# Kernel tuning notes

Hardware: AMD Instinct MI355X
Metric: run time of the kernel (lower is better)

Reference implementation:

```python
import jax, jax.numpy as jnp
import numpy as np

B, C1, C2 = 8, 256, 256
Cc = 128          # c = int(c2 * e)
RED = 16          # reduction in FrequencyModulation
HEADS = 8
HD = Cc // HEADS  # 16
HH, WW = 32, 32


def _c1x1(x, w, b=None):
    # 1x1 conv as channel contraction; w: [out_c, in_c]
    y = jnp.einsum('bchw,oc->bohw', x, w)
    return y if b is None else y + b[None, :, None, None]


def setup_inputs() -> dict:
    key = jax.random.key(0)
    ks = jax.random.split(key, 22)
    s = 0.02
    p = {}
    p['x'] = jax.random.normal(ks[0], (B, C1, HH, WW), jnp.float32)
    p['cv1_w'] = jax.random.normal(ks[1], (2 * Cc, C1), jnp.float32) * s
    p['cv1_b'] = jnp.zeros((2 * Cc,), jnp.float32)
    # FrequencyModulation params
    p['fm_w1'] = jax.random.normal(ks[2], (Cc // RED, Cc), jnp.float32) * s
    p['fm_w2'] = jax.random.normal(ks[3], (Cc, Cc // RED), jnp.float32) * s
    p['ca_w1'] = jax.random.normal(ks[4], (Cc // RED, Cc), jnp.float32) * s
    p['ca_w2'] = jax.random.normal(ks[5], (Cc, Cc // RED), jnp.float32) * s
    # TokenStatisticsSelfAttention params (qkv_bias=False)
    p['qkv_w'] = jax.random.normal(ks[6], (3 * Cc, Cc), jnp.float32) * s
    p['tproj_w'] = jax.random.normal(ks[7], (Cc, Cc), jnp.float32) * s
    p['tproj_b'] = jnp.zeros((Cc,), jnp.float32)
    # SpatialQuantizedRouter params
    p['dw_w'] = jax.random.normal(ks[8], (Cc, 1, 3, 3), jnp.float32) * s  # depthwise
    p['dw_b'] = jnp.zeros((Cc,), jnp.float32)
    p['rt_w'] = jax.random.normal(ks[9], (1, Cc), jnp.float32) * s
    p['rt_b'] = jnp.zeros((1,), jnp.float32)
    p['q_w'] = jax.random.normal(ks[10], (Cc, Cc), jnp.float32) * s
    p['k_w'] = jax.random.normal(ks[11], (Cc, Cc), jnp.float32) * s
    p['v_w'] = jax.random.normal(ks[12], (Cc, Cc), jnp.float32) * s
    p['sproj_w'] = jax.random.normal(ks[13], (Cc, Cc), jnp.float32) * s
    p['sproj_b'] = jnp.zeros((Cc,), jnp.float32)
    p['cv2_w'] = jax.random.normal(ks[14], (C2, 3 * Cc), jnp.float32) * s
    p['cv2_b'] = jnp.zeros((C2,), jnp.float32)
    return p


def _forward(x, cv1_w, cv1_b, fm_w1, fm_w2, ca_w1, ca_w2, qkv_w, tproj_w,
             tproj_b, dw_w, dw_b, rt_w, rt_b, q_w, k_w, v_w, sproj_w,
             sproj_b, cv2_w, cv2_b):
    Bb, _, H, W = x.shape
    N = H * W
    y = _c1x1(x, cv1_w, cv1_b)
    y0, y1 = y[:, :Cc], y[:, Cc:]

    # ---- Branch 1: FrequencyModulation ----
    xf = jnp.fft.rfft2(y1.astype(jnp.float32), norm='ortho')  # [B,c,H,W//2+1] complex
    mag = jnp.abs(xf)
    pooled = mag.mean(axis=(-2, -1))                          # [B,c]
    fw = jax.nn.sigmoid(jax.nn.relu(pooled @ fm_w1.T) @ fm_w2.T)  # [B,c]
    # mag*fw*exp(i*phase) == fw * xf  (fw is real, per batch/channel)
    xs = jnp.fft.irfft2(xf * fw[:, :, None, None].astype(jnp.complex64),
                        s=(H, W), norm='ortho')               # [B,c,H,W]
    ca = jax.nn.sigmoid(jax.nn.relu(xs.mean(axis=(-2, -1)) @ ca_w1.T) @ ca_w2.T)
    freq_out = xs * ca[:, :, None, None]

    # ---- Branch 2: TokenStatisticsSelfAttention ----
    xt = y1.reshape(Bb, Cc, N).transpose(0, 2, 1)             # [B,N,c]
    qkv = (xt @ qkv_w.T).reshape(Bb, N, 3, HEADS, HD).transpose(2, 0, 3, 1, 4)
    q, k, v = qkv[0], qkv[1], qkv[2]                          # [B,h,N,d]
    var_v = jnp.var(v, axis=-1, ddof=1, keepdims=True)        # [B,h,N,1] (unbiased)
    var_k = jnp.var(k, axis=-1, ddof=1, keepdims=True)
    attn = jax.nn.softmax(jnp.einsum('bhnx,bhmx->bhnm', var_v, var_k) * (HD ** -0.5), axis=-1)
    to = jnp.einsum('bhnm,bhmd->bhnd', attn, v).transpose(0, 2, 1, 3).reshape(Bb, N, Cc)
    stat_out = ((to @ tproj_w.T) + tproj_b).transpose(0, 2, 1).reshape(Bb, Cc, H, W)

    # ---- Branch 3: SpatialQuantizedRouter (training-mode blend) ----
    x_local = jax.lax.conv_general_dilated(
        y1, dw_w, (1, 1), 'SAME', feature_group_count=Cc,
        dimension_numbers=('NCHW', 'OIHW', 'NCHW')) + dw_b[None, :, None, None]
    p_route = jax.nn.sigmoid(y1.mean(axis=(-2, -1)) @ rt_w.T + rt_b)  # [B,1]
    qb = jnp.sign(_c1x1(y1, q_w).reshape(Bb, Cc, N))
    kb = jnp.sign(_c1x1(y1, k_w).reshape(Bb, Cc, N))
    vv = _c1x1(y1, v_w).reshape(Bb, Cc, N)
    a2 = jax.nn.softmax(jnp.einsum('bcn,bcm->bnm', qb, kb) * (Cc ** -0.5), axis=-1)
    # torch: bmm(v, attn.T) -> out[b,c,n] = sum_m v[b,c,m]*attn[b,n,m]
    ob = jnp.einsum('bcm,bnm->bcn', vv, a2).reshape(Bb, Cc, H, W)
    out_bin = _c1x1(ob, sproj_w, sproj_b)
    alpha = p_route.reshape(Bb, 1, 1, 1)
    spat_out = (1.0 - alpha) * x_local + alpha * out_bin

    attn_out = freq_out + stat_out + spat_out
    yc = jnp.concatenate([y0, y1, attn_out], axis=1)          # [B,3c,H,W]
    out = _c1x1(yc, cv2_w, cv2_b)
    return x + out  # add: shortcut and c1 == c2


def reference(x, cv1_w, cv1_b, fm_w1, fm_w2, ca_w1, ca_w2, qkv_w, tproj_w,
              tproj_b, dw_w, dw_b, rt_w, rt_b, q_w, k_w, v_w, sproj_w,
              sproj_b, cv2_w, cv2_b):
    return _forward(x, cv1_w, cv1_b, fm_w1, fm_w2, ca_w1, ca_w2, qkv_w,
                    tproj_w, tproj_b, dw_w, dw_b, rt_w, rt_b, q_w, k_w, v_w,
                    sproj_w, sproj_b, cv2_w, cv2_b)
```

## Files before the change

### kernel.cpp

```cpp
#include <hip/hip_runtime.h>
#include <math.h>

#define BATCH 8
#define NPIX 1024

typedef __attribute__((ext_vector_type(8))) short short8v;
typedef __attribute__((ext_vector_type(4))) float f32x4;

__device__ inline unsigned short f2bf(float x) {
  unsigned int u = __float_as_uint(x);
  return (unsigned short)((u + 0x7FFFu + ((u >> 16) & 1u)) >> 16);
}
__device__ inline float bf2f(unsigned short h) {
  return __uint_as_float((unsigned int)h << 16);
}
__device__ inline unsigned long long pack4bf(float a, float b, float c, float d) {
  return (unsigned long long)(unsigned short)f2bf(a) |
         ((unsigned long long)(unsigned short)f2bf(b) << 16) |
         ((unsigned long long)(unsigned short)f2bf(c) << 32) |
         ((unsigned long long)(unsigned short)f2bf(d) << 48);
}

__global__ __launch_bounds__(256) void convw_kernel(
    const float* __restrict__ cv1_w, const float* __restrict__ qkv_w,
    const float* __restrict__ tproj_w, const float* __restrict__ sproj_w,
    const float* __restrict__ cv2_w, const float* __restrict__ q_w,
    const float* __restrict__ k_w, const float* __restrict__ v_w,
    short* __restrict__ wb) {
  int i = blockIdx.x * 256 + threadIdx.x;
  float v;
  if (i < 65536) v = cv1_w[i];
  else if (i < 163840) {
    int j = i - 65536;
    if (j < 49152) v = qkv_w[j];
    else {
      int jj = j - 49152, wsel = jj >> 14, r = jj & 16383;
      v = (wsel == 0) ? q_w[r] : (wsel == 1) ? k_w[r] : v_w[r];
    }
  }
  else if (i < 180224) v = tproj_w[i - 163840];
  else if (i < 196608) v = sproj_w[i - 180224];
  else v = cv2_w[i - 196608];
  wb[i] = (short)f2bf(v);
}

template<int MODE, bool HAS_BIAS, bool HAS_RES, bool XF32T, bool EMIT_HI>
__global__ __launch_bounds__(256) void mgemm_kernel(
    const short* __restrict__ Wb, const void* __restrict__ Xsrc, int ldx,
    const float* __restrict__ bias, const float* __restrict__ res,
    void* __restrict__ Y0, void* __restrict__ Y1,
    int K, long sXT, long sY, long sR, int tStride, int tOff) {
  __shared__ __align__(16) short As[64][40];
  __shared__ __align__(16) short Bs[64][40];
  const int b = blockIdx.z;
  const int n0 = blockIdx.x * 64, m0 = blockIdx.y * 64;
  const int tid = threadIdx.x;
  const int l = tid & 63, w = tid >> 6;
  const int wm = w >> 1, wn = w & 1;
  const int sr = tid >> 2, sko = (tid & 3) * 8;
  const int xr = tid >> 3, xcg = (tid & 7) * 8;
  const int fr = l & 15, fk = (l >> 4) * 8;
  f32x4 acc[2][2] = {};
  for (int k0 = 0; k0 < K; k0 += 32) {
    *(uint4*)&As[sr][sko] = *(const uint4*)(Wb + (long)(m0 + sr) * K + k0 + sko);
    if (XF32T) {
      const float* Xf = (const float*)Xsrc + (long)b * sXT;
      const float4 xa = *(const float4*)(Xf + (long)(k0 + xr) * 1024 + n0 + xcg);
      const float4 xb = *(const float4*)(Xf + (long)(k0 + xr) * 1024 + n0 + xcg + 4);
      Bs[xcg + 0][xr] = (short)f2bf(xa.x); Bs[xcg + 1][xr] = (short)f2bf(xa.y);
      Bs[xcg + 2][xr] = (short)f2bf(xa.z); Bs[xcg + 3][xr] = (short)f2bf(xa.w);
      Bs[xcg + 4][xr] = (short)f2bf(xb.x); Bs[xcg + 5][xr] = (short)f2bf(xb.y);
      Bs[xcg + 6][xr] = (short)f2bf(xb.z); Bs[xcg + 7][xr] = (short)f2bf(xb.w);
    } else {
      const short* Xb = (const short*)Xsrc + (long)b * sXT;
      *(uint4*)&Bs[sr][sko] = *(const uint4*)(Xb + (long)(n0 + sr) * ldx + k0 + sko);
    }
    __syncthreads();
    short8v a0 = *(short8v*)&As[wm * 32 + fr][fk];
    short8v a1 = *(short8v*)&As[wm * 32 + 16 + fr][fk];
    short8v b0 = *(short8v*)&Bs[wn * 32 + fr][fk];
    short8v b1 = *(short8v*)&Bs[wn * 32 + 16 + fr][fk];
    acc[0][0] = __builtin_amdgcn_mfma_f32_16x16x32_bf16(a0, b0, acc[0][0], 0, 0, 0);
    acc[0][1] = __builtin_amdgcn_mfma_f32_16x16x32_bf16(a0, b1, acc[0][1], 0, 0, 0);
    acc[1][0] = __builtin_amdgcn_mfma_f32_16x16x32_bf16(a1, b0, acc[1][0], 0, 0, 0);
    acc[1][1] = __builtin_amdgcn_mfma_f32_16x16x32_bf16(a1, b1, acc[1][1], 0, 0, 0);
    __syncthreads();
  }
#pragma unroll
  for (int tm = 0; tm < 2; tm++) {
    const int m_base = m0 + wm * 32 + tm * 16 + (l >> 4) * 4;
#pragma unroll
    for (int tn = 0; tn < 2; tn++) {
      const int n = n0 + wn * 32 + tn * 16 + (l & 15);
      float v0 = acc[tm][tn][0], v1 = acc[tm][tn][1];
      float v2 = acc[tm][tn][2], v3 = acc[tm][tn][3];
      if (HAS_BIAS) {
        v0 += bias[m_base]; v1 += bias[m_base + 1];
        v2 += bias[m_base + 2]; v3 += bias[m_base + 3];
      }
      if (HAS_RES) {
        v0 += res[(long)b * sR + (long)(m_base + 0) * 1024 + n];
        v1 += res[(long)b * sR + (long)(m_base + 1) * 1024 + n];
        v2 += res[(long)b * sR + (long)(m_base + 2) * 1024 + n];
        v3 += res[(long)b * sR + (long)(m_base + 3) * 1024 + n];
      }
      if (MODE == 0) {
        float* Y = (float*)Y0 + (long)b * sY + n;
        Y[(long)(m_base + 0) * 1024] = v0; Y[(long)(m_base + 1) * 1024] = v1;
        Y[(long)(m_base + 2) * 1024] = v2; Y[(long)(m_base + 3) * 1024] = v3;
      } else if (MODE == 1) {
        short* Y = (short*)Y0 + (long)b * sY + n;
        Y[(long)(m_base + 0) * 1024] = (short)f2bf(v0);
        Y[(long)(m_base + 1) * 1024] = (short)f2bf(v1);
        Y[(long)(m_base + 2) * 1024] = (short)f2bf(v2);
        Y[(long)(m_base + 3) * 1024] = (short)f2bf(v3);
      } else if (MODE == 2) {
        *(unsigned long long*)((short*)Y0 + ((long)b * 1024 + n) * tStride +
                               tOff + m_base) = pack4bf(v0, v1, v2, v3);
        if (EMIT_HI && m_base >= 128) {
          float* Y = (float*)Y1 + ((long)b * 128 + m_base - 128) * 1024 + n;
          Y[0] = v0; Y[1024] = v1; Y[2048] = v2; Y[3072] = v3;
        }
      } else {
        if (m0 < 384) {
          float* Y = (float*)Y0 + (long)b * 384 * 1024 + (long)m_base * 1024 + n;
          Y[0] = v0; Y[1024] = v1; Y[2048] = v2; Y[3072] = v3;
        } else {
          *(unsigned long long*)((short*)Y1 + ((long)b * 1024 + n) * 384 +
                                 (m_base - 384)) = pack4bf(v0, v1, v2, v3);
        }
      }
    }
  }
}

__global__ __launch_bounds__(256) void fftpool_kernel(
    const float* __restrict__ y1, float* __restrict__ pooled, float* __restrict__ m1) {
  const int bc = blockIdx.x;
  const float* img = y1 + (long)bc * NPIX;
  __shared__ float im[1024];
  __shared__ float Gr[32][17], Gi[32][17];
  __shared__ float cs[32], sn[32];
  __shared__ float red[256];
  const int t = threadIdx.x;
  if (t < 32) {
    float ang = -0.19634954084936207f * (float)t;
    __sincosf(ang, &sn[t], &cs[t]);
  }
  float lsum = 0.f;
  for (int i = t; i < 1024; i += 256) { float v = img[i]; im[i] = v; lsum += v; }
  red[t] = lsum;
  __syncthreads();
  for (int s = 128; s > 0; s >>= 1) {
    if (t < s) red[t] += red[t + s];
    __syncthreads();
  }
  if (t == 0) m1[bc] = red[0] * (1.f / 1024.f);
  for (int i = t; i < 544; i += 256) {
    int h = i / 17, v = i % 17;
    float ar = 0.f, ai = 0.f;
    for (int w2 = 0; w2 < 32; w2++) {
      int k = (v * w2) & 31;
      float x = im[h * 32 + w2];
      ar += x * cs[k]; ai += x * sn[k];
    }
    Gr[h][v] = ar; Gi[h][v] = ai;
  }
  __syncthreads();
  float asum = 0.f;
  for (int i = t; i < 544; i += 256) {
    int u = i / 17, v = i % 17;
    float xr = 0.f, xi = 0.f;
    for (int h = 0; h < 32; h++) {
      int k = (u * h) & 31;
      float gr = Gr[h][v], gi = Gi[h][v];
      xr += gr * cs[k] - gi * sn[k];
      xi += gr * sn[k] + gi * cs[k];
    }
    asum += sqrtf(xr * xr + xi * xi);
  }
  red[t] = asum;
  __syncthreads();
  for (int s = 128; s > 0; s >>= 1) {
    if (t < s) red[t] += red[t + s];
    __syncthreads();
  }
  if (t == 0) pooled[bc] = red[0] * (1.f / (32.f * 544.f));
}

__global__ __launch_bounds__(128) void gates_kernel(
    const float* __restrict__ pooled, const float* __restrict__ m1,
    const float* __restrict__ fm_w1, const float* __restrict__ fm_w2,
    const float* __restrict__ ca_w1, const float* __restrict__ ca_w2,
    const float* __restrict__ rt_w, const float* __restrict__ rt_b,
    float* __restrict__ g, float* __restrict__ alpha) {
  const int b = blockIdx.x, t = threadIdx.x;
  __shared__ float h1[8], fwv[128], xsm[128], h2[8];
  const float* pb = pooled + b * 128;
  const float* mb = m1 + b * 128;
  if (t < 8) {
    float s = 0.f;
    for (int c = 0; c < 128; c++) s += pb[c] * fm_w1[t * 128 + c];
    h1[t] = fmaxf(s, 0.f);
  }
  __syncthreads();
  {
    float s = 0.f;
    for (int r = 0; r < 8; r++) s += h1[r] * fm_w2[t * 8 + r];
    float fw = 1.f / (1.f + __expf(-s));
    fwv[t] = fw; xsm[t] = fw * mb[t];
  }
  __syncthreads();
  if (t < 8) {
    float s = 0.f;
    for (int c = 0; c < 128; c++) s += xsm[c] * ca_w1[t * 128 + c];
    h2[t] = fmaxf(s, 0.f);
  }
  __syncthreads();
  {
    float s = 0.f;
    for (int r = 0; r < 8; r++) s += h2[r] * ca_w2[t * 8 + r];
    float ca = 1.f / (1.f + __expf(-s));
    g[b * 128 + t] = fwv[t] * ca;
  }
  if (t == 0) {
    float s = 0.f;
    for (int c = 0; c < 128; c++) s += mb[c] * rt_w[c];
    s += rt_b[0];
    alpha[b] = 1.f / (1.f + __expf(-s));
  }
}

__global__ __launch_bounds__(256) void varmax_kernel(
    const float* __restrict__ qkvb, float* __restrict__ var_k,
    float* __restrict__ var_v, float* __restrict__ maxvk,
    short* __restrict__ vTb) {
  const int bh = blockIdx.x;
  const int b = bh >> 3, h = bh & 7;
  __shared__ float red[256];
  __shared__ float trans[16][256];
  const float* kb = qkvb + ((long)b * 384 + 128 + h * 16) * NPIX;
  const float* vb = qkvb + ((long)b * 384 + 256 + h * 16) * NPIX;
  float mx = 0.f;
  for (int j = 0; j < 4; j++) {
    int n = threadIdx.x + j * 256;
    float xk[16], xv[16], sk = 0.f, sv = 0.f;
#pragma unroll
    for (int d = 0; d < 16; d++) {
      xk[d] = kb[(long)d * NPIX + n]; sk += xk[d];
      xv[d] = vb[(long)d * NPIX + n]; sv += xv[d];
    }
    float mk = sk * (1.f / 16.f), mv = sv * (1.f / 16.f);
    float vk_ = 0.f, vv_ = 0.f;
#pragma unroll
    for (int d = 0; d < 16; d++) {
      float a = xk[d] - mk; vk_ += a * a;
      float c = xv[d] - mv; vv_ += c * c;
    }
    vk_ *= (1.f / 15.f); vv_ *= (1.f / 15.f);
    var_k[(long)bh * NPIX + n] = vk_;
    var_v[(long)bh * NPIX + n] = vv_;
    mx = fmaxf(mx, vk_);
#pragma unroll
    for (int d = 0; d < 16; d++) trans[d][threadIdx.x] = xv[d];
    __syncthreads();
    {
      int d = threadIdx.x >> 4, mc = threadIdx.x & 15;
      __align__(16) short tmp[16];
#pragma unroll
      for (int e = 0; e < 16; e++) tmp[e] = (short)f2bf(trans[d][mc * 16 + e]);
      short* dst = vTb + ((long)bh * 16 + d) * 1024 + j * 256 + mc * 16;
      *(uint4*)dst = *(uint4*)tmp;
      *(uint4*)(dst + 8) = *(uint4*)(tmp + 8);
    }
    __syncthreads();
  }
  red[threadIdx.x] = mx;
  __syncthreads();
  for (int s = 128; s > 0; s >>= 1) {
    if (threadIdx.x < s) red[threadIdx.x] = fmaxf(red[threadIdx.x], red[threadIdx.x + s]);
    __syncthreads();
  }
  if (threadIdx.x == 0) maxvk[bh] = red[0];
}

__global__ __launch_bounds__(256) void stat_mfma_kernel(
    const short* __restrict__ vTb, const float* __restrict__ var_k,
    const float* __restrict__ var_v, const float* __restrict__ maxvk,
    short* __restrict__ tcT) {
  const int bh = blockIdx.x;
  const int b = bh >> 3, h = bh & 7;
  const int n0 = blockIdx.y * 64;
  const int tid = threadIdx.x;
  const int l = tid & 63, w = tid >> 6;
  const int ln = l & 15, lk = l >> 4;
  const int n = n0 + w * 16 + ln;
  __shared__ float vk[1024];
  for (int i = tid; i < 1024; i += 256) vk[i] = var_k[(long)bh * 1024 + i];
  const float cn = var_v[(long)bh * 1024 + n] * 0.25f;
  const float mv = maxvk[bh];
  const short* arow = vTb + ((long)bh * 16 + ln) * 1024 + lk * 8;
  __syncthreads();
  f32x4 acc = {};
  float psum = 0.f;
  for (int m0 = 0; m0 < 1024; m0 += 32) {
    short8v afrag = *(const short8v*)(arow + m0);
    short8v bfrag;
#pragma unroll
    for (int j = 0; j < 8; j++) {
      float wv = __expf(cn * (vk[m0 + lk * 8 + j] - mv));
      psum += wv;
      bfrag[j] = (short)f2bf(wv);
    }
    acc = __builtin_amdgcn_mfma_f32_16x16x32_bf16(afrag, bfrag, acc, 0, 0, 0);
  }
  psum += __shfl_xor(psum, 16);
  psum += __shfl_xor(psum, 32);
  const float inv = 1.f / psum;
  *(unsigned long long*)(tcT + ((long)b * 1024 + n) * 128 + h * 16 + lk * 4) =
      pack4bf(acc[0] * inv, acc[1] * inv, acc[2] * inv, acc[3] * inv);
}

__global__ __launch_bounds__(256) void pack_kernel(
    const short* __restrict__ sqkvT,
    unsigned long long* __restrict__ qbits, unsigned long long* __restrict__ kbits) {
  const int wave = threadIdx.x >> 6, lane = threadIdx.x & 63;
  const long p = (long)blockIdx.x * 4 + wave;
  const short* base = sqkvT + p * 384;
  unsigned long long q0 = __ballot(bf2f((unsigned short)base[lane]) > 0.f);
  unsigned long long q1 = __ballot(bf2f((unsigned short)base[64 + lane]) > 0.f);
  unsigned long long k0 = __ballot(bf2f((unsigned short)base[128 + lane]) > 0.f);
  unsigned long long k1 = __ballot(bf2f((unsigned short)base[192 + lane]) > 0.f);
  if (lane == 0) {
    qbits[p * 2] = q0; qbits[p * 2 + 1] = q1;
    kbits[p * 2] = k0; kbits[p * 2 + 1] = k1;
  }
}

__global__ __launch_bounds__(256) void obgemm_kernel(
    const short* __restrict__ pvb, const unsigned long long* __restrict__ qbits,
    const unsigned long long* __restrict__ kbits, short* __restrict__ pnum,
    float* __restrict__ pden) {
  const int b = blockIdx.z;
  const int sp = blockIdx.y;
  const int n0 = blockIdx.x * 64;
  const int kb0 = sp * 256;
  __shared__ __align__(16) short As[128][40];
  __shared__ __align__(16) unsigned long long kbsh[256][2];
  const int tid = threadIdx.x;
  const int l = tid & 63, w = tid >> 6;
  const int ln = l & 15, lk = l >> 4;
  const int n = n0 + w * 16 + ln;
  const unsigned long long q0 = qbits[((long)b * 1024 + n) * 2];
  const unsigned long long q1 = qbits[((long)b * 1024 + n) * 2 + 1];
  *(uint4*)&kbsh[tid][0] = *(const uint4*)(kbits + ((long)b * 1024 + kb0 + tid) * 2);
  const float fs = 0.08838834764831845f;
  const int sc = tid >> 1, sh = (tid & 1) * 16;
  const short* pvrow = pvb + ((long)b * 128 + sc) * 1024 + kb0;
  f32x4 acc[8] = {};
  float psum = 0.f;
  for (int ks = 0; ks < 8; ks++) {
    *(uint4*)&As[sc][sh] = *(const uint4*)(pvrow + ks * 32 + sh);
    *(uint4*)&As[sc][sh + 8] = *(const uint4*)(pvrow + ks * 32 + sh + 8);
    __syncthreads();
    const int mloc = ks * 32 + lk * 8;
    short8v bfrag;
#pragma unroll
    for (int j = 0; j < 8; j++) {
      unsigned long long kw0 = kbsh[mloc + j][0];
      unsigned long long kw1 = kbsh[mloc + j][1];
      int ham = __popcll(kw0 ^ q0) + __popcll(kw1 ^ q1);
      float wv = __expf((float)(128 - 2 * ham) * fs);
      psum += wv;
      bfrag[j] = (short)f2bf(wv);
    }
#pragma unroll
    for (int ct = 0; ct < 8; ct++) {
      short8v afrag = *(short8v*)&As[ct * 16 + ln][lk * 8];
      acc[ct] = __builtin_amdgcn_mfma_f32_16x16x32_bf16(afrag, bfrag, acc[ct], 0, 0, 0);
    }
    __syncthreads();
  }
  short* dst = pnum + (((long)sp * 8 + b) * 128) * 1024 + n;
#pragma unroll
  for (int ct = 0; ct < 8; ct++)
#pragma unroll
    for (int i = 0; i < 4; i++)
      dst[(long)(ct * 16 + lk * 4 + i) * 1024] = (short)f2bf(acc[ct][i]);
  psum += __shfl_xor(psum, 16);
  psum += __shfl_xor(psum, 32);
  if (lk == 0)
    pden[((long)sp * 8 + b) * 1024 + n] = psum;
}

__global__ __launch_bounds__(256) void dwcombine_kernel(
    const float* __restrict__ y1, float* __restrict__ attn,
    const float* __restrict__ dw_w, const float* __restrict__ dw_b,
    const short* __restrict__ pnum, const float* __restrict__ pden,
    const float* __restrict__ sproj_b, const float* __restrict__ g,
    const float* __restrict__ alpha) {
  const int bc = blockIdx.x;
  const int b = bc >> 7, cx = bc & 127;
  const float* img = y1 + (long)bc * NPIX;
  float* dst = attn + (long)bc * NPIX;
  float w[9];
#pragma unroll
  for (int i = 0; i < 9; i++) w[i] = dw_w[cx * 9 + i];
  const float bias = dw_b[cx];
  const float a = alpha[b];
  const float gg = g[bc];
  const float sb = sproj_b[cx];
  const long ns = 8L * 128 * 1024;
  const long ds = 8L * 1024;
  const long nbase = (long)bc * 1024;
  const long dbase = (long)b * 1024;
  for (int i = threadIdx.x; i < 1024; i += 256) {
    int h = i >> 5, wx = i & 31;
    float s = bias;
#pragma unroll
    for (int ky = 0; ky < 3; ky++) {
      int hh = h + ky - 1;
      if (hh < 0 || hh > 31) continue;
#pragma unroll
      for (int kx = 0; kx < 3; kx++) {
        int ww2 = wx + kx - 1;
        if (ww2 < 0 || ww2 > 31) continue;
        s += img[hh * 32 + ww2] * w[ky * 3 + kx];
      }
    }
    float num = bf2f((unsigned short)pnum[nbase + i]) +
                bf2f((unsigned short)pnum[nbase + i + ns]) +
                bf2f((unsigned short)pnum[nbase + i + 2 * ns]) +
                bf2f((unsigned short)pnum[nbase + i + 3 * ns]);
    float den = pden[dbase + i] + pden[dbase + i + ds] +
                pden[dbase + i + 2 * ds] + pden[dbase + i + 3 * ds];
    float obv = num / den + sb;
    dst[i] = gg * img[i] + (1.f - a) * s + a * obv;
  }
}

extern "C" void kernel_launch(void* const* d_in, const int* in_sizes, int n_in,
                              void* d_out, int out_size, void* d_ws, size_t ws_size,
                              hipStream_t stream) {
  const float* x = (const float*)d_in[0];
  const float* cv1_w = (const float*)d_in[1];
  const float* cv1_b = (const float*)d_in[2];
  const float* fm_w1 = (const float*)d_in[3];
  const float* fm_w2 = (const float*)d_in[4];
  const float* ca_w1 = (const float*)d_in[5];
  const float* ca_w2 = (const float*)d_in[6];
  const float* qkv_w = (const float*)d_in[7];
  const float* tproj_w = (const float*)d_in[8];
  const float* tproj_b = (const float*)d_in[9];
  const float* dw_w = (const float*)d_in[10];
  const float* dw_b = (const float*)d_in[11];
  const float* rt_w = (const float*)d_in[12];
  const float* rt_b = (const float*)d_in[13];
  const float* q_w = (const float*)d_in[14];
  const float* k_w = (const float*)d_in[15];
  const float* v_w = (const float*)d_in[16];
  const float* sproj_w = (const float*)d_in[17];
  const float* sproj_b = (const float*)d_in[18];
  const float* cv2_w = (const float*)d_in[19];
  const float* cv2_b = (const float*)d_in[20];
  float* out = (float*)d_out;

  char* wsp = (char*)d_ws;
  size_t off = 0;
  auto alloc = [&](size_t bytes) {
    void* p = wsp + off;
    off += (bytes + 255) & ~(size_t)255;
    return p;
  };
  float* qkvb = (float*)alloc(8UL * 384 * 1024 * 4);
  float* y1 = (float*)alloc(8UL * 128 * 1024 * 4);
  float* attn = (float*)alloc(8UL * 128 * 1024 * 4);
  short* ycT = (short*)alloc(8UL * 1024 * 384 * 2);
  short* sqkvT = (short*)alloc(8UL * 1024 * 384 * 2);
  short* tcT = (short*)alloc(8UL * 1024 * 128 * 2);
  short* pvb = (short*)alloc(8UL * 128 * 1024 * 2);
  short* wb = (short*)alloc(294912UL * 2);
  short* vTb = (short*)alloc(64UL * 16 * 1024 * 2);
  float* pden = (float*)alloc(4UL * 8 * 1024 * 4);
  float* var_k = (float*)alloc(8UL * 8 * 1024 * 4);
  float* var_v = (float*)alloc(8UL * 8 * 1024 * 4);
  float* maxvk = (float*)alloc(64 * 4);
  float* pooled = (float*)alloc(1024 * 4);
  float* m1 = (float*)alloc(1024 * 4);
  float* g = (float*)alloc(1024 * 4);
  float* alpha = (float*)alloc(8 * 4);
  unsigned long long* qbits = (unsigned long long*)alloc(8192UL * 2 * 8);
  unsigned long long* kbits = (unsigned long long*)alloc(8192UL * 2 * 8);
  short* pnum = (short*)qkvb;
  const short* cv1b = wb;
  const short* qsb = wb + 65536;
  const short* tprojb = wb + 163840;
  const short* sprojb = wb + 180224;
  const short* cv2b = wb + 196608;
  if (off > ws_size) return;

  dim3 blk(256);
  convw_kernel<<<dim3(1152), blk, 0, stream>>>(cv1_w, qkv_w, tproj_w, sproj_w,
                                               cv2_w, q_w, k_w, v_w, wb);
  mgemm_kernel<2, true, false, true, true><<<dim3(16, 4, 8), blk, 0, stream>>>(
      cv1b, x, 0, cv1_b, nullptr, ycT, y1, 256, 256L * 1024, 0, 0, 384, 0);
  fftpool_kernel<<<dim3(1024), blk, 0, stream>>>(y1, pooled, m1);
  gates_kernel<<<dim3(8), dim3(128), 0, stream>>>(pooled, m1, fm_w1, fm_w2,
                                                  ca_w1, ca_w2, rt_w, rt_b, g, alpha);
  mgemm_kernel<3, false, false, false, false><<<dim3(16, 12, 8), blk, 0, stream>>>(
      qsb, ycT + 128, 384, nullptr, nullptr, qkvb, sqkvT, 128, 1024L * 384,
      0, 0, 0, 0);
  varmax_kernel<<<dim3(64), blk, 0, stream>>>(qkvb, var_k, var_v, maxvk, vTb);
  stat_mfma_kernel<<<dim3(64, 16), blk, 0, stream>>>(vTb, var_k, var_v, maxvk, tcT);
  pack_kernel<<<dim3(2048), blk, 0, stream>>>(sqkvT, qbits, kbits);
  mgemm_kernel<1, false, false, false, false><<<dim3(16, 2, 8), blk, 0, stream>>>(
      sprojb, sqkvT + 256, 384, nullptr, nullptr, pvb, nullptr, 128,
      1024L * 384, 128L * 1024, 0, 0, 0);
  obgemm_kernel<<<dim3(16, 4, 8), blk, 0, stream>>>(pvb, qbits, kbits, pnum, pden);
  dwcombine_kernel<<<dim3(1024), blk, 0, stream>>>(y1, attn, dw_w, dw_b, pnum,
                                                   pden, sproj_b, g, alpha);
  mgemm_kernel<2, true, true, false, false><<<dim3(16, 2, 8), blk, 0, stream>>>(
      tprojb, tcT, 128, tproj_b, attn, ycT, nullptr, 128, 1024L * 128, 0,
      128L * 1024, 384, 256);
  mgemm_kernel<0, true, true, false, false><<<dim3(16, 4, 8), blk, 0, stream>>>(
      cv2b, ycT, 384, cv2_b, x, out, nullptr, 384, 1024L * 384, 256L * 1024,
      256L * 1024, 0, 0);
}
```

Measured before the change: 123.0 us.

## Fuse weight conversion, depthwise combine, and split varmax across more blocks

Removes the standalone weight-conversion kernel. Most GEMMs now convert fp32 weights to bf16 while loading tiles, and the qkv/q/k/v conversion is folded into the FFT pooling kernel. The depthwise-conv and attention-combine kernel is fused into the epilogue of the tproj GEMM, which drops the fp32 attn intermediate and one launch. varmax is split into 4 chunks per head with an atomicMax reduction, and gates_kernel zeroes the max buffer. The cost is redundant per-tile weight conversion, a heavier epilogue doing scattered 3x3 loads, and reliance on atomicMax over float bits, which is valid only because variances are non-negative.

```diff
diff --git a/kernel.cpp b/kernel.cpp
--- a/kernel.cpp
+++ b/kernel.cpp
@@ -21,35 +21,16 @@
          ((unsigned long long)(unsigned short)f2bf(d) << 48);
 }
 
-__global__ __launch_bounds__(256) void convw_kernel(
-    const float* __restrict__ cv1_w, const float* __restrict__ qkv_w,
-    const float* __restrict__ tproj_w, const float* __restrict__ sproj_w,
-    const float* __restrict__ cv2_w, const float* __restrict__ q_w,
-    const float* __restrict__ k_w, const float* __restrict__ v_w,
-    short* __restrict__ wb) {
-  int i = blockIdx.x * 256 + threadIdx.x;
-  float v;
-  if (i < 65536) v = cv1_w[i];
-  else if (i < 163840) {
-    int j = i - 65536;
-    if (j < 49152) v = qkv_w[j];
-    else {
-      int jj = j - 49152, wsel = jj >> 14, r = jj & 16383;
-      v = (wsel == 0) ? q_w[r] : (wsel == 1) ? k_w[r] : v_w[r];
-    }
-  }
-  else if (i < 180224) v = tproj_w[i - 163840];
-  else if (i < 196608) v = sproj_w[i - 180224];
-  else v = cv2_w[i - 196608];
-  wb[i] = (short)f2bf(v);
-}
-
-template<int MODE, bool HAS_BIAS, bool HAS_RES, bool XF32T, bool EMIT_HI>
+template<int MODE, bool HAS_BIAS, bool HAS_RES, bool XF32T, bool WF32, bool EMIT_HI>
 __global__ __launch_bounds__(256) void mgemm_kernel(
-    const short* __restrict__ Wb, const void* __restrict__ Xsrc, int ldx,
+    const void* __restrict__ Wsrc, const void* __restrict__ Xsrc, int ldx,
     const float* __restrict__ bias, const float* __restrict__ res,
     void* __restrict__ Y0, void* __restrict__ Y1,
-    int K, long sXT, long sY, long sR, int tStride, int tOff) {
+    int K, long sXT, long sY, long sR, int tStride, int tOff,
+    const float* __restrict__ y1p, const short* __restrict__ pnumS,
+    const float* __restrict__ pdenP, const float* __restrict__ sproj_bP,
+    const float* __restrict__ dw_wP, const float* __restrict__ dw_bP,
+    const float* __restrict__ gP, const float* __restrict__ alphaP) {
   __shared__ __align__(16) short As[64][40];
   __shared__ __align__(16) short Bs[64][40];
   const int b = blockIdx.z;
@@ -62,7 +43,18 @@
   const int fr = l & 15, fk = (l >> 4) * 8;
   f32x4 acc[2][2] = {};
   for (int k0 = 0; k0 < K; k0 += 32) {
-    *(uint4*)&As[sr][sko] = *(const uint4*)(Wb + (long)(m0 + sr) * K + k0 + sko);
+    if (WF32) {
+      const float* Wf = (const float*)Wsrc;
+      const float4 wa = *(const float4*)(Wf + (long)(m0 + sr) * K + k0 + sko);
+      const float4 wbv = *(const float4*)(Wf + (long)(m0 + sr) * K + k0 + sko + 4);
+      As[sr][sko + 0] = (short)f2bf(wa.x); As[sr][sko + 1] = (short)f2bf(wa.y);
+      As[sr][sko + 2] = (short)f2bf(wa.z); As[sr][sko + 3] = (short)f2bf(wa.w);
+      As[sr][sko + 4] = (short)f2bf(wbv.x); As[sr][sko + 5] = (short)f2bf(wbv.y);
+      As[sr][sko + 6] = (short)f2bf(wbv.z); As[sr][sko + 7] = (short)f2bf(wbv.w);
+    } else {
+      *(uint4*)&As[sr][sko] =
+          *(const uint4*)((const short*)Wsrc + (long)(m0 + sr) * K + k0 + sko);
+    }
     if (XF32T) {
       const float* Xf = (const float*)Xsrc + (long)b * sXT;
       const float4 xa = *(const float4*)(Xf + (long)(k0 + xr) * 1024 + n0 + xcg);
@@ -121,7 +113,7 @@
           float* Y = (float*)Y1 + ((long)b * 128 + m_base - 128) * 1024 + n;
           Y[0] = v0; Y[1024] = v1; Y[2048] = v2; Y[3072] = v3;
         }
-      } else {
+      } else if (MODE == 3) {
         if (m0 < 384) {
           float* Y = (float*)Y0 + (long)b * 384 * 1024 + (long)m_base * 1024 + n;
           Y[0] = v0; Y[1024] = v1; Y[2048] = v2; Y[3072] = v3;
@@ -129,20 +121,72 @@
           *(unsigned long long*)((short*)Y1 + ((long)b * 1024 + n) * 384 +
                                  (m_base - 384)) = pack4bf(v0, v1, v2, v3);
         }
+      } else {
+        const float aab = alphaP[b];
+        const long ds_ = 8L * 1024;
+        const long dbase = (long)b * 1024 + n;
+        const float den = pdenP[dbase] + pdenP[dbase + ds_] +
+                          pdenP[dbase + 2 * ds_] + pdenP[dbase + 3 * ds_];
+        const long ns_ = 8L * 128 * 1024;
+        const int hh = n >> 5, wc = n & 31;
+        float tv[4] = {v0, v1, v2, v3};
+        float outv[4];
+#pragma unroll
+        for (int i = 0; i < 4; i++) {
+          int c = m_base + i;
+          const float* img = y1p + ((long)b * 128 + c) * 1024;
+          float s = dw_bP[c];
+#pragma unroll
+          for (int ky = 0; ky < 3; ky++) {
+            int h2 = hh + ky - 1;
+            if (h2 < 0 || h2 > 31) continue;
+#pragma unroll
+            for (int kx = 0; kx < 3; kx++) {
+              int w2 = wc + kx - 1;
+              if (w2 < 0 || w2 > 31) continue;
+              s += img[h2 * 32 + w2] * dw_wP[c * 9 + ky * 3 + kx];
+            }
+          }
+          long nb = ((long)b * 128 + c) * 1024 + n;
+          float num = bf2f((unsigned short)pnumS[nb]) +
+                      bf2f((unsigned short)pnumS[nb + ns_]) +
+                      bf2f((unsigned short)pnumS[nb + 2 * ns_]) +
+                      bf2f((unsigned short)pnumS[nb + 3 * ns_]);
+          float obv = num / den + sproj_bP[c];
+          outv[i] = tv[i] + gP[b * 128 + c] * img[n] + (1.f - aab) * s + aab * obv;
+        }
+        *(unsigned long long*)((short*)Y0 + ((long)b * 1024 + n) * tStride +
+                               tOff + m_base) =
+            pack4bf(outv[0], outv[1], outv[2], outv[3]);
       }
     }
   }
 }
 
 __global__ __launch_bounds__(256) void fftpool_kernel(
-    const float* __restrict__ y1, float* __restrict__ pooled, float* __restrict__ m1) {
+    const float* __restrict__ y1, float* __restrict__ pooled, float* __restrict__ m1,
+    const float* __restrict__ qkv_w, const float* __restrict__ q_w,
+    const float* __restrict__ k_w, const float* __restrict__ v_w,
+    short* __restrict__ qarena) {
   const int bc = blockIdx.x;
+  const int t = threadIdx.x;
+  {
+    int gid = bc * 256 + t;
+    if (gid < 98304) {
+      float v;
+      if (gid < 49152) v = qkv_w[gid];
+      else {
+        int jj = gid - 49152, wsel = jj >> 14, r = jj & 16383;
+        v = (wsel == 0) ? q_w[r] : (wsel == 1) ? k_w[r] : v_w[r];
+      }
+      qarena[gid] = (short)f2bf(v);
+    }
+  }
   const float* img = y1 + (long)bc * NPIX;
   __shared__ float im[1024];
   __shared__ float Gr[32][17], Gi[32][17];
   __shared__ float cs[32], sn[32];
   __shared__ float red[256];
-  const int t = threadIdx.x;
   if (t < 32) {
     float ang = -0.19634954084936207f * (float)t;
     __sincosf(ang, &sn[t], &cs[t]);
@@ -193,9 +237,10 @@
     const float* __restrict__ fm_w1, const float* __restrict__ fm_w2,
     const float* __restrict__ ca_w1, const float* __restrict__ ca_w2,
     const float* __restrict__ rt_w, const float* __restrict__ rt_b,
-    float* __restrict__ g, float* __restrict__ alpha) {
+    float* __restrict__ g, float* __restrict__ alpha, float* __restrict__ maxvk) {
   const int b = blockIdx.x, t = threadIdx.x;
   __shared__ float h1[8], fwv[128], xsm[128], h2[8];
+  if (t < 8) maxvk[b * 8 + t] = 0.f;
   const float* pb = pooled + b * 128;
   const float* mb = m1 + b * 128;
   if (t < 8) {
@@ -236,52 +281,49 @@
     float* __restrict__ var_v, float* __restrict__ maxvk,
     short* __restrict__ vTb) {
   const int bh = blockIdx.x;
+  const int chunk = blockIdx.y;
   const int b = bh >> 3, h = bh & 7;
   __shared__ float red[256];
   __shared__ float trans[16][256];
+  const int n = chunk * 256 + threadIdx.x;
   const float* kb = qkvb + ((long)b * 384 + 128 + h * 16) * NPIX;
   const float* vb = qkvb + ((long)b * 384 + 256 + h * 16) * NPIX;
-  float mx = 0.f;
-  for (int j = 0; j < 4; j++) {
-    int n = threadIdx.x + j * 256;
-    float xk[16], xv[16], sk = 0.f, sv = 0.f;
-#pragma unroll
-    for (int d = 0; d < 16; d++) {
-      xk[d] = kb[(long)d * NPIX + n]; sk += xk[d];
-      xv[d] = vb[(long)d * NPIX + n]; sv += xv[d];
-    }
-    float mk = sk * (1.f / 16.f), mv = sv * (1.f / 16.f);
-    float vk_ = 0.f, vv_ = 0.f;
-#pragma unroll
-    for (int d = 0; d < 16; d++) {
-      float a = xk[d] - mk; vk_ += a * a;
-      float c = xv[d] - mv; vv_ += c * c;
-    }
-    vk_ *= (1.f / 15.f); vv_ *= (1.f / 15.f);
-    var_k[(long)bh * NPIX + n] = vk_;
-    var_v[(long)bh * NPIX + n] = vv_;
-    mx = fmaxf(mx, vk_);
-#pragma unroll
-    for (int d = 0; d < 16; d++) trans[d][threadIdx.x] = xv[d];
-    __syncthreads();
-    {
-      int d = threadIdx.x >> 4, mc = threadIdx.x & 15;
-      __align__(16) short tmp[16];
-#pragma unroll
-      for (int e = 0; e < 16; e++) tmp[e] = (short)f2bf(trans[d][mc * 16 + e]);
-      short* dst = vTb + ((long)bh * 16 + d) * 1024 + j * 256 + mc * 16;
-      *(uint4*)dst = *(uint4*)tmp;
-      *(uint4*)(dst + 8) = *(uint4*)(tmp + 8);
-    }
-    __syncthreads();
-  }
-  red[threadIdx.x] = mx;
+  float xk[16], xv[16], sk = 0.f, sv = 0.f;
+#pragma unroll
+  for (int d = 0; d < 16; d++) {
+    xk[d] = kb[(long)d * NPIX + n]; sk += xk[d];
+    xv[d] = vb[(long)d * NPIX + n]; sv += xv[d];
+  }
+  float mk = sk * (1.f / 16.f), mv = sv * (1.f / 16.f);
+  float vk_ = 0.f, vv_ = 0.f;
+#pragma unroll
+  for (int d = 0; d < 16; d++) {
+    float a = xk[d] - mk; vk_ += a * a;
+    float c = xv[d] - mv; vv_ += c * c;
+  }
+  vk_ *= (1.f / 15.f); vv_ *= (1.f / 15.f);
+  var_k[(long)bh * NPIX + n] = vk_;
+  var_v[(long)bh * NPIX + n] = vv_;
+#pragma unroll
+  for (int d = 0; d < 16; d++) trans[d][threadIdx.x] = xv[d];
+  __syncthreads();
+  {
+    int d = threadIdx.x >> 4, mc = threadIdx.x & 15;
+    __align__(16) short tmp[16];
+#pragma unroll
+    for (int e = 0; e < 16; e++) tmp[e] = (short)f2bf(trans[d][mc * 16 + e]);
+    short* dst = vTb + ((long)bh * 16 + d) * 1024 + chunk * 256 + mc * 16;
+    *(uint4*)dst = *(uint4*)tmp;
+    *(uint4*)(dst + 8) = *(uint4*)(tmp + 8);
+  }
+  red[threadIdx.x] = vk_;
   __syncthreads();
   for (int s = 128; s > 0; s >>= 1) {
     if (threadIdx.x < s) red[threadIdx.x] = fmaxf(red[threadIdx.x], red[threadIdx.x + s]);
     __syncthreads();
   }
-  if (threadIdx.x == 0) maxvk[bh] = red[0];
+  if (threadIdx.x == 0)
+    atomicMax((int*)(maxvk + bh), __float_as_int(red[0]));
 }
 
 __global__ __launch_bounds__(256) void stat_mfma_kernel(
@@ -393,52 +435,6 @@
     pden[((long)sp * 8 + b) * 1024 + n] = psum;
 }
 
-__global__ __launch_bounds__(256) void dwcombine_kernel(
-    const float* __restrict__ y1, float* __restrict__ attn,
-    const float* __restrict__ dw_w, const float* __restrict__ dw_b,
-    const short* __restrict__ pnum, const float* __restrict__ pden,
-    const float* __restrict__ sproj_b, const float* __restrict__ g,
-    const float* __restrict__ alpha) {
-  const int bc = blockIdx.x;
-  const int b = bc >> 7, cx = bc & 127;
-  const float* img = y1 + (long)bc * NPIX;
-  float* dst = attn + (long)bc * NPIX;
-  float w[9];
-#pragma unroll
-  for (int i = 0; i < 9; i++) w[i] = dw_w[cx * 9 + i];
-  const float bias = dw_b[cx];
-  const float a = alpha[b];
-  const float gg = g[bc];
-  const float sb = sproj_b[cx];
-  const long ns = 8L * 128 * 1024;
-  const long ds = 8L * 1024;
-  const long nbase = (long)bc * 1024;
-  const long dbase = (long)b * 1024;
-  for (int i = threadIdx.x; i < 1024; i += 256) {
-    int h = i >> 5, wx = i & 31;
-    float s = bias;
-#pragma unroll
-    for (int ky = 0; ky < 3; ky++) {
-      int hh = h + ky - 1;
-      if (hh < 0 || hh > 31) continue;
-#pragma unroll
-      for (int kx = 0; kx < 3; kx++) {
-        int ww2 = wx + kx - 1;
-        if (ww2 < 0 || ww2 > 31) continue;
-        s += img[hh * 32 + ww2] * w[ky * 3 + kx];
-      }
-    }
-    float num = bf2f((unsigned short)pnum[nbase + i]) +
-                bf2f((unsigned short)pnum[nbase + i + ns]) +
-                bf2f((unsigned short)pnum[nbase + i + 2 * ns]) +
-                bf2f((unsigned short)pnum[nbase + i + 3 * ns]);
-    float den = pden[dbase + i] + pden[dbase + i + ds] +
-                pden[dbase + i + 2 * ds] + pden[dbase + i + 3 * ds];
-    float obv = num / den + sb;
-    dst[i] = gg * img[i] + (1.f - a) * s + a * obv;
-  }
-}
-
 extern "C" void kernel_launch(void* const* d_in, const int* in_sizes, int n_in,
                               void* d_out, int out_size, void* d_ws, size_t ws_size,
                               hipStream_t stream) {
@@ -474,12 +470,11 @@
   };
   float* qkvb = (float*)alloc(8UL * 384 * 1024 * 4);
   float* y1 = (float*)alloc(8UL * 128 * 1024 * 4);
-  float* attn = (float*)alloc(8UL * 128 * 1024 * 4);
   short* ycT = (short*)alloc(8UL * 1024 * 384 * 2);
   short* sqkvT = (short*)alloc(8UL * 1024 * 384 * 2);
   short* tcT = (short*)alloc(8UL * 1024 * 128 * 2);
   short* pvb = (short*)alloc(8UL * 128 * 1024 * 2);
-  short* wb = (short*)alloc(294912UL * 2);
+  short* qarena = (short*)alloc(98304UL * 2);
   short* vTb = (short*)alloc(64UL * 16 * 1024 * 2);
   float* pden = (float*)alloc(4UL * 8 * 1024 * 4);
   float* var_k = (float*)alloc(8UL * 8 * 1024 * 4);
@@ -492,37 +487,34 @@
   unsigned long long* qbits = (unsigned long long*)alloc(8192UL * 2 * 8);
   unsigned long long* kbits = (unsigned long long*)alloc(8192UL * 2 * 8);
   short* pnum = (short*)qkvb;
-  const short* cv1b = wb;
-  const short* qsb = wb + 65536;
-  const short* tprojb = wb + 163840;
-  const short* sprojb = wb + 180224;
-  const short* cv2b = wb + 196608;
   if (off > ws_size) return;
 
   dim3 blk(256);
-  convw_kernel<<<dim3(1152), blk, 0, stream>>>(cv1_w, qkv_w, tproj_w, sproj_w,
-                                               cv2_w, q_w, k_w, v_w, wb);
-  mgemm_kernel<2, true, false, true, true><<<dim3(16, 4, 8), blk, 0, stream>>>(
-      cv1b, x, 0, cv1_b, nullptr, ycT, y1, 256, 256L * 1024, 0, 0, 384, 0);
-  fftpool_kernel<<<dim3(1024), blk, 0, stream>>>(y1, pooled, m1);
+  mgemm_kernel<2, true, false, true, true, true><<<dim3(16, 4, 8), blk, 0, stream>>>(
+      cv1_w, x, 0, cv1_b, nullptr, ycT, y1, 256, 256L * 1024, 0, 0, 384, 0,
+      nullptr, nullptr, nullptr, nullptr, nullptr, nullptr, nullptr, nullptr);
+  fftpool_kernel<<<dim3(1024), blk, 0, stream>>>(y1, pooled, m1, qkv_w, q_w,
+                                                 k_w, v_w, qarena);
   gates_kernel<<<dim3(8), dim3(128), 0, stream>>>(pooled, m1, fm_w1, fm_w2,
-                                                  ca_w1, ca_w2, rt_w, rt_b, g, alpha);
-  mgemm_kernel<3, false, false, false, false><<<dim3(16, 12, 8), blk, 0, stream>>>(
-      qsb, ycT + 128, 384, nullptr, nullptr, qkvb, sqkvT, 128, 1024L * 384,
-      0, 0, 0, 0);
-  varmax_kernel<<<dim3(64), blk, 0, stream>>>(qkvb, var_k, var_v, maxvk, vTb);
+                                                  ca_w1, ca_w2, rt_w, rt_b, g,
+                                                  alpha, maxvk);
+  mgemm_kernel<3, false, false, false, false, false><<<dim3(16, 12, 8), blk, 0, stream>>>(
+      qarena, ycT + 128, 384, nullptr, nullptr, qkvb, sqkvT, 128, 1024L * 384,
+      0, 0, 0, 0, nullptr, nullptr, nullptr, nullptr, nullptr, nullptr,
+      nullptr, nullptr);
+  varmax_kernel<<<dim3(64, 4), blk, 0, stream>>>(qkvb, var_k, var_v, maxvk, vTb);
   stat_mfma_kernel<<<dim3(64, 16), blk, 0, stream>>>(vTb, var_k, var_v, maxvk, tcT);
   pack_kernel<<<dim3(2048), blk, 0, stream>>>(sqkvT, qbits, kbits);
-  mgemm_kernel<1, false, false, false, false><<<dim3(16, 2, 8), blk, 0, stream>>>(
-      sprojb, sqkvT + 256, 384, nullptr, nullptr, pvb, nullptr, 128,
-      1024L * 384, 128L * 1024, 0, 0, 0);
+  mgemm_kernel<1, false, false, false, true, false><<<dim3(16, 2, 8), blk, 0, stream>>>(
+      sproj_w, sqkvT + 256, 384, nullptr, nullptr, pvb, nullptr, 128,
+      1024L * 384, 128L * 1024, 0, 0, 0, nullptr, nullptr, nullptr, nullptr,
+      nullptr, nullptr, nullptr, nullptr);
   obgemm_kernel<<<dim3(16, 4, 8), blk, 0, stream>>>(pvb, qbits, kbits, pnum, pden);
-  dwcombine_kernel<<<dim3(1024), blk, 0, stream>>>(y1, attn, dw_w, dw_b, pnum,
-                                                   pden, sproj_b, g, alpha);
-  mgemm_kernel<2, true, true, false, false><<<dim3(16, 2, 8), blk, 0, stream>>>(
-      tprojb, tcT, 128, tproj_b, attn, ycT, nullptr, 128, 1024L * 128, 0,
-      128L * 1024, 384, 256);
-  mgemm_kernel<0, true, true, false, false><<<dim3(16, 4, 8), blk, 0, stream>>>(
-      cv2b, ycT, 384, cv2_b, x, out, nullptr, 384, 1024L * 384, 256L * 1024,
-      256L * 1024, 0, 0);
-}
+  mgemm_kernel<4, true, false, false, true, false><<<dim3(16, 2, 8), blk, 0, stream>>>(
+      tproj_w, tcT, 128, tproj_b, nullptr, ycT, nullptr, 128, 1024L * 128, 0,
+      0, 384, 256, y1, pnum, pden, sproj_b, dw_w, dw_b, g, alpha);
+  mgemm_kernel<0, true, true, false, true, false><<<dim3(16, 4, 8), blk, 0, stream>>>(
+      cv2_w, ycT, 384, cv2_b, x, out, nullptr, 384, 1024L * 384, 256L * 1024,
+      256L * 1024, 0, 0, nullptr, nullptr, nullptr, nullptr, nullptr, nullptr,
+      nullptr, nullptr);
+}
```

New measurement: 128.0 us. 4.1% more time.
